# Optimization experiments

Hardware: AMD Instinct MI355X
Metric: run time of the kernel (lower is better)

Reference implementation:

```python
import jax, jax.numpy as jnp
import numpy as np

EPS = 1e-5

def bn(x, g, b):
    # BatchNorm1d, training-mode batch statistics.
    axes = (0, 2) if x.ndim == 3 else (0,)
    m = jnp.mean(x, axis=axes, keepdims=True)
    v = jnp.var(x, axis=axes, keepdims=True)
    shape = (1, -1, 1) if x.ndim == 3 else (1, -1)
    return (x - m) / jnp.sqrt(v + EPS) * g.reshape(shape) + b.reshape(shape)

def conv1(x, w):
    # 1x1 conv1d == channel matmul: w [O,C], x [B,C,N]
    return jnp.einsum('oc,bcn->bon', w, x)

def knn_cov(x, local_idx, k):
    # x: [B,C,N], local_idx: [B,N] bool (local=True branch)
    B, C, N = x.shape
    xx = jnp.sum(x * x, axis=1, keepdims=True)          # [B,1,N]
    inner = -2.0 * jnp.einsum('bcn,bcm->bnm', x, x)      # [B,N,N]
    pd = -xx - inner - jnp.swapaxes(xx, 1, 2)            # neg sq dist [B,N,N]
    Min = jnp.min(pd, axis=-1)                           # [B,N]
    pd = jnp.where(local_idx[:, None, :], pd, Min[:, :, None])
    idx = jax.lax.top_k(jax.lax.stop_gradient(pd), k)[1]  # [B,N,k] nearest
    pts = jnp.swapaxes(x, 1, 2)                          # [B,N,C]
    knn_x = jax.vmap(lambda p, i: p[i])(pts, idx)        # [B,N,k,C]
    knn_x = knn_x - jnp.mean(knn_x, axis=2, keepdims=True)
    cov = jnp.einsum('bnkc,bnkd->bncd', knn_x, knn_x)    # [B,N,C,C]
    cov = cov.reshape(B, N, C * C).transpose(0, 2, 1)    # [B,C^2,N]
    return jnp.concatenate([x, cov], axis=1)             # [B,C+C^2,N]

def setup_inputs() -> dict:
    key = jax.random.key(0)
    ks = jax.random.split(key, 16)
    B, C, N, k = 4, 3, 8192, 20
    emb = 1024
    d = {}
    d['x'] = jax.random.normal(ks[0], (B, C, N), dtype=jnp.float32)
    d['local_idx'] = jax.random.randint(ks[1], (B, N), 0, 2) > 0
    d['k'] = k
    cin = C + C * C  # 12
    d['w1'] = jax.random.normal(ks[2], (64, cin), jnp.float32) * 0.1
    d['w2'] = jax.random.normal(ks[3], (64, 64), jnp.float32) * 0.1
    d['w3'] = jax.random.normal(ks[4], (64, 64), jnp.float32) * 0.1
    d['w4'] = jax.random.normal(ks[5], (128, 64), jnp.float32) * 0.1
    d['w5'] = jax.random.normal(ks[6], (emb, 128), jnp.float32) * 0.05
    for i, c in zip(range(1, 6), [64, 64, 64, 128, emb]):
        d[f'g{i}'] = jnp.ones((c,), jnp.float32)
        d[f'b{i}'] = jnp.zeros((c,), jnp.float32)
    d['lw1'] = jax.random.normal(ks[7], (512, emb), jnp.float32) * 0.03
    d['g6'] = jnp.ones((512,), jnp.float32)
    d['b6'] = jnp.zeros((512,), jnp.float32)
    d['lw2'] = jax.random.normal(ks[8], (4, 512), jnp.float32) * 0.05
    d['lb2'] = jnp.zeros((4,), jnp.float32)
    return d

def reference(x, local_idx, k, w1, w2, w3, w4, w5,
              g1, b1, g2, b2, g3, b3, g4, b4, g5, b5,
              lw1, g6, b6, lw2, lb2):
    h = knn_cov(x, local_idx, k)                 # [B,12,N]
    h = jax.nn.relu(bn(conv1(h, w1), g1, b1))
    h = jax.nn.relu(bn(conv1(h, w2), g2, b2))
    h = jax.nn.relu(bn(conv1(h, w3), g3, b3))
    h = jax.nn.relu(bn(conv1(h, w4), g4, b4))
    h = jax.nn.relu(bn(conv1(h, w5), g5, b5))    # [B,emb,N]
    h = jnp.max(h, axis=2)                        # global max pool [B,emb]
    h = jax.nn.relu(bn(h @ lw1.T, g6, b6))        # [B,512]
    # dropout: identity at eval
    return h @ lw2.T + lb2                        # [B,4]
```

## Files before the change

kernel.cpp:

```cpp
#include <hip/hip_runtime.h>

constexpr int BB = 4, NN = 8192, KNB = 20;
constexpr int BN_ = BB * NN;
constexpr float EPSV = 1e-5f;

constexpr size_t OFF_MODE  = 0;
constexpr size_t OFF_PCNT  = 16;
constexpr size_t OFF_PL    = 64;
constexpr size_t OFF_M0 = OFF_PL + 131072;
constexpr size_t OFF_S0 = OFF_M0 + 12;
constexpr size_t OFF_M1 = OFF_S0 + 144;
constexpr size_t OFF_S1 = OFF_M1 + 64;
constexpr size_t OFF_M2 = OFF_S1 + 64 * 64;
constexpr size_t OFF_S2 = OFF_M2 + 64;
constexpr size_t OFF_M3 = OFF_S2 + 64 * 64;
constexpr size_t OFF_S3 = OFF_M3 + 64;
constexpr size_t OFF_M4 = OFF_S3 + 64 * 64;
constexpr size_t OFF_S4 = OFF_M4 + 128;
constexpr size_t OFF_POOL = OFF_S4 + 128 * 128;
constexpr size_t OFF_ZEND = OFF_POOL + BB * 1024;
constexpr size_t OFF_A1 = OFF_ZEND;
constexpr size_t OFF_B1 = OFF_A1 + 64;
constexpr size_t OFF_A2 = OFF_B1 + 64;
constexpr size_t OFF_B2 = OFF_A2 + 64;
constexpr size_t OFF_A3 = OFF_B2 + 64;
constexpr size_t OFF_B3 = OFF_A3 + 64;
constexpr size_t OFF_A4 = OFF_B3 + 64;
constexpr size_t OFF_B4 = OFF_A4 + 128;
constexpr size_t OFF_A5 = OFF_B4 + 128;
constexpr size_t OFF_B5 = OFF_A5 + 1024;
constexpr size_t OFF_SH = OFF_B5 + 1024;
constexpr size_t OFF_WT1 = OFF_SH + BB * 512;
constexpr size_t OFF_WT2 = OFF_WT1 + 768;
constexpr size_t OFF_WT3 = OFF_WT2 + 4096;
constexpr size_t OFF_WT4 = OFF_WT3 + 4096;
constexpr size_t OFF_WT5_RAW = OFF_WT4 + 8192;
constexpr size_t OFF_WT5 = (OFF_WT5_RAW + 63) & ~size_t(63);
constexpr size_t OFF_H0_RAW = OFF_WT5 + 1024 * 128;
constexpr size_t OFF_H0 = (OFF_H0_RAW + 63) & ~size_t(63);
constexpr size_t OFF_H1 = OFF_H0 + (size_t)BB * 12 * NN;
constexpr size_t OFF_H2 = OFF_H1 + (size_t)BB * 64 * NN;
constexpr size_t OFF_H3 = OFF_H1;
constexpr size_t OFF_H4 = OFF_H2 + (size_t)BB * 64 * NN;
constexpr size_t OFF_P64  = OFF_H4;
constexpr size_t OFF_P128 = OFF_H1;
constexpr size_t WS_FLOATS = OFF_H4 + (size_t)BB * 128 * NN;

__device__ inline float dist3(const float4 c, float x0, float x1, float x2) {
  const float d0 = c.x - x0, d1 = c.y - x1, d2 = c.z - x2;
  return __builtin_fmaf(d0, d0, __builtin_fmaf(d1, d1, d2 * d2));
}

__global__ __launch_bounds__(256) void k_prep(const unsigned int* __restrict__ li32,
                                              int* __restrict__ mode,
                                              int* __restrict__ pcnt,
                                              float4* __restrict__ pl,
                                              const float* __restrict__ x) {
  const int b = blockIdx.x;
  const int t = threadIdx.x;
  const int lane = t & 63;
  const int w = t >> 6;
  __shared__ int s_wc[4];
  __shared__ int s_base;
  __shared__ int s_any;
  if (t == 0) { s_base = 0; s_any = 0; }
  __syncthreads();
  unsigned int any = 0;
  for (int i = t; i < 2048; i += 256) any |= (li32[b * 2048 + i] > 1u) ? 1u : 0u;
  if (any) atomicOr(&s_any, 1);
  __syncthreads();
  const int md = s_any;
  if (b == 0 && t == 0) *mode = md;
  const unsigned char* p8 = (const unsigned char*)li32;
  const float* __restrict__ xb = x + (size_t)b * 3 * NN;
  for (int j0 = 0; j0 < NN; j0 += 256) {
    const int m = j0 + t;
    const int f = md ? (p8[b * NN + m] != 0) : (li32[b * NN + m] != 0);
    const unsigned long long mask = __ballot(f);
    const int pos = __popcll(mask & ((1ull << lane) - 1ull));
    if (lane == 0) s_wc[w] = (int)__popcll(mask);
    __syncthreads();
    int off = s_base;
    for (int ww = 0; ww < w; ++ww) off += s_wc[ww];
    const int tot = s_wc[0] + s_wc[1] + s_wc[2] + s_wc[3];
    if (f) pl[(size_t)b * NN + off + pos] =
        make_float4(xb[m], xb[NN + m], xb[2 * NN + m], __int_as_float(m));
    __syncthreads();
    if (t == 0) s_base += tot;
    __syncthreads();
  }
  if (t == 0) pcnt[b] = s_base;
}

__global__ void k_wtall(const float* __restrict__ w1, const float* __restrict__ w2,
                        const float* __restrict__ w3, const float* __restrict__ w4,
                        const float* __restrict__ w5, float* __restrict__ wt1,
                        float* __restrict__ wt2, float* __restrict__ wt3,
                        float* __restrict__ wt4, float* __restrict__ wt5) {
  const int i = blockIdx.x * 256 + threadIdx.x;
  if (i < 768)        { const int o = i / 12,  c = i % 12;  wt1[c * 64 + o]  = w1[i]; }
  else if (i < 4864)  { const int j = i - 768;  const int o = j >> 6, c = j & 63;  wt2[c * 64 + o]  = w2[j]; }
  else if (i < 8960)  { const int j = i - 4864; const int o = j >> 6, c = j & 63;  wt3[c * 64 + o]  = w3[j]; }
  else if (i < 17152) { const int j = i - 8960; const int o = j >> 6, c = j & 63;  wt4[c * 128 + o] = w4[j]; }
  else if (i < 148224){ const int j = i - 17152;const int o = j >> 7, c = j & 127; wt5[c * 1024 + o] = w5[j]; }
}

__global__ __launch_bounds__(512) void k_knn(const float* __restrict__ x,
                                             const float4* __restrict__ pl,
                                             const int* __restrict__ pcnt,
                                             float* __restrict__ h0) {
  const int blk  = blockIdx.x;
  const int b    = blk >> 7;
  const int tile = blk & 127;
  const int t    = threadIdx.x;
  const int lane = t & 63;
  const int w    = __builtin_amdgcn_readfirstlane(t >> 6);
  const int n    = tile * 64 + lane;

  __shared__ float s_pool[8 * 64 * 21];
  __shared__ float s_T[64];
  __shared__ float s_red[64][13];
  __shared__ int   s_tc[64];
  __shared__ int   s_ti[64][24];
  float* __restrict__ s_dbuf = s_pool;

  const float* __restrict__ xb  = x + (size_t)b * 3 * NN;
  const float4* __restrict__ plb = pl + (size_t)b * NN;
  const int cnt = pcnt[b];
  const float xn0 = xb[n], xn1 = xb[NN + n], xn2 = xb[2 * NN + n];

  const int jlo = (cnt * w) >> 3;
  const int jhi = (cnt * (w + 1)) >> 3;

  float tk[KNB];
#pragma unroll
  for (int i = 0; i < KNB; ++i) tk[i] = 3.0e38f;

  {
    float thr = 3.0e38f;
    int bc = 0;
    int j = jlo;
    for (; j + 3 < jhi; j += 4) {
      const float4 c0 = plb[j],     c1 = plb[j + 1];
      const float4 c2 = plb[j + 2], c3 = plb[j + 3];
      const float d0 = dist3(c0, xn0, xn1, xn2);
      const float d1 = dist3(c1, xn0, xn1, xn2);
      const float d2 = dist3(c2, xn0, xn1, xn2);
      const float d3 = dist3(c3, xn0, xn1, xn2);
      if (d0 < thr) { s_dbuf[bc * 512 + t] = d0; ++bc; }
      if (d1 < thr) { s_dbuf[bc * 512 + t] = d1; ++bc; }
      if (d2 < thr) { s_dbuf[bc * 512 + t] = d2; ++bc; }
      if (d3 < thr) { s_dbuf[bc * 512 + t] = d3; ++bc; }
      if (__any(bc >= 8)) {
        for (int i = 0; i < bc; ++i) {
          float dv = s_dbuf[i * 512 + t];
          if (dv < tk[KNB - 1]) {
#pragma unroll
            for (int q2 = 0; q2 < KNB; ++q2) {
              const float lo = fminf(tk[q2], dv);
              dv = fmaxf(tk[q2], dv);
              tk[q2] = lo;
            }
          }
        }
        bc = 0;
        thr = tk[KNB - 1];
      }
    }
    for (; j < jhi; ++j) {
      const float4 c = plb[j];
      const float d = dist3(c, xn0, xn1, xn2);
      if (d < thr) { s_dbuf[bc * 512 + t] = d; ++bc; }
    }
    for (int i = 0; i < bc; ++i) {
      float dv = s_dbuf[i * 512 + t];
      if (dv < tk[KNB - 1]) {
#pragma unroll
        for (int q2 = 0; q2 < KNB; ++q2) {
          const float lo = fminf(tk[q2], dv);
          dv = fmaxf(tk[q2], dv);
          tk[q2] = lo;
        }
      }
    }
  }
  __syncthreads();

  {
    const int base = (w * 64 + lane) * 21;
#pragma unroll
    for (int i = 0; i < KNB; ++i) s_pool[base + i] = tk[i];
    s_pool[base + KNB] = 3.0e38f;
  }
  __syncthreads();

  if (w == 0) {
    int i0 = 0, i1 = 0, i2 = 0, i3 = 0, i4 = 0, i5 = 0, i6 = 0, i7 = 0;
    float T = 0.f;
    for (int c = 0; c < KNB; ++c) {
      const float v0 = s_pool[(0 * 64 + lane) * 21 + i0];
      const float v1 = s_pool[(1 * 64 + lane) * 21 + i1];
      const float v2 = s_pool[(2 * 64 + lane) * 21 + i2];
      const float v3 = s_pool[(3 * 64 + lane) * 21 + i3];
      const float v4 = s_pool[(4 * 64 + lane) * 21 + i4];
      const float v5 = s_pool[(5 * 64 + lane) * 21 + i5];
      const float v6 = s_pool[(6 * 64 + lane) * 21 + i6];
      const float v7 = s_pool[(7 * 64 + lane) * 21 + i7];
      float best = fminf(fminf(fminf(v0, v1), fminf(v2, v3)),
                         fminf(fminf(v4, v5), fminf(v6, v7)));
      int adv, taken;
      adv = (v0 == best) ? 1 : 0;           i0 += adv; taken = adv;
      adv = (!taken && v1 == best) ? 1 : 0; i1 += adv; taken |= adv;
      adv = (!taken && v2 == best) ? 1 : 0; i2 += adv; taken |= adv;
      adv = (!taken && v3 == best) ? 1 : 0; i3 += adv; taken |= adv;
      adv = (!taken && v4 == best) ? 1 : 0; i4 += adv; taken |= adv;
      adv = (!taken && v5 == best) ? 1 : 0; i5 += adv; taken |= adv;
      adv = (!taken && v6 == best) ? 1 : 0; i6 += adv; taken |= adv;
      adv = (!taken && v7 == best) ? 1 : 0; i7 += adv;
      T = best;
    }
    s_T[lane] = T;
    s_tc[lane] = 0;
  }
  __syncthreads();
  const float T = s_T[lane];

  float sx = 0, sy = 0, sz = 0;
  float xx = 0, xy = 0, xz = 0, yy = 0, yz = 0, zz = 0;
  float clf = 0;
  {
    int j = jlo;
    for (; j + 3 < jhi; j += 4) {
      const float4 c0 = plb[j],     c1 = plb[j + 1];
      const float4 c2 = plb[j + 2], c3 = plb[j + 3];
      const float d0 = dist3(c0, xn0, xn1, xn2);
      const float d1 = dist3(c1, xn0, xn1, xn2);
      const float d2 = dist3(c2, xn0, xn1, xn2);
      const float d3 = dist3(c3, xn0, xn1, xn2);
      if (d0 < T) {
        clf += 1.f; sx += c0.x; sy += c0.y; sz += c0.z;
        xx = __builtin_fmaf(c0.x, c0.x, xx); xy = __builtin_fmaf(c0.x, c0.y, xy);
        xz = __builtin_fmaf(c0.x, c0.z, xz); yy = __builtin_fmaf(c0.y, c0.y, yy);
        yz = __builtin_fmaf(c0.y, c0.z, yz); zz = __builtin_fmaf(c0.z, c0.z, zz);
      } else if (d0 == T) {
        const int pos = atomicAdd(&s_tc[lane], 1);
        if (pos < 24) s_ti[lane][pos] = j;
      }
      if (d1 < T) {
        clf += 1.f; sx += c1.x; sy += c1.y; sz += c1.z;
        xx = __builtin_fmaf(c1.x, c1.x, xx); xy = __builtin_fmaf(c1.x, c1.y, xy);
        xz = __builtin_fmaf(c1.x, c1.z, xz); yy = __builtin_fmaf(c1.y, c1.y, yy);
        yz = __builtin_fmaf(c1.y, c1.z, yz); zz = __builtin_fmaf(c1.z, c1.z, zz);
      } else if (d1 == T) {
        const int pos = atomicAdd(&s_tc[lane], 1);
        if (pos < 24) s_ti[lane][pos] = j + 1;
      }
      if (d2 < T) {
        clf += 1.f; sx += c2.x; sy += c2.y; sz += c2.z;
        xx = __builtin_fmaf(c2.x, c2.x, xx); xy = __builtin_fmaf(c2.x, c2.y, xy);
        xz = __builtin_fmaf(c2.x, c2.z, xz); yy = __builtin_fmaf(c2.y, c2.y, yy);
        yz = __builtin_fmaf(c2.y, c2.z, yz); zz = __builtin_fmaf(c2.z, c2.z, zz);
      } else if (d2 == T) {
        const int pos = atomicAdd(&s_tc[lane], 1);
        if (pos < 24) s_ti[lane][pos] = j + 2;
      }
      if (d3 < T) {
        clf += 1.f; sx += c3.x; sy += c3.y; sz += c3.z;
        xx = __builtin_fmaf(c3.x, c3.x, xx); xy = __builtin_fmaf(c3.x, c3.y, xy);
        xz = __builtin_fmaf(c3.x, c3.z, xz); yy = __builtin_fmaf(c3.y, c3.y, yy);
        yz = __builtin_fmaf(c3.y, c3.z, yz); zz = __builtin_fmaf(c3.z, c3.z, zz);
      } else if (d3 == T) {
        const int pos = atomicAdd(&s_tc[lane], 1);
        if (pos < 24) s_ti[lane][pos] = j + 3;
      }
    }
    for (; j < jhi; ++j) {
      const float4 c = plb[j];
      const float d = dist3(c, xn0, xn1, xn2);
      if (d < T) {
        clf += 1.f; sx += c.x; sy += c.y; sz += c.z;
        xx = __builtin_fmaf(c.x, c.x, xx); xy = __builtin_fmaf(c.x, c.y, xy);
        xz = __builtin_fmaf(c.x, c.z, xz); yy = __builtin_fmaf(c.y, c.y, yy);
        yz = __builtin_fmaf(c.y, c.z, yz); zz = __builtin_fmaf(c.z, c.z, zz);
      } else if (d == T) {
        const int pos = atomicAdd(&s_tc[lane], 1);
        if (pos < 24) s_ti[lane][pos] = j;
      }
    }
  }
  __syncthreads();
  {
    const int base = (w * 64 + lane) * 13;
    s_pool[base + 0] = sx; s_pool[base + 1] = sy; s_pool[base + 2] = sz;
    s_pool[base + 3] = xx; s_pool[base + 4] = xy; s_pool[base + 5] = xz;
    s_pool[base + 6] = yy; s_pool[base + 7] = yz; s_pool[base + 8] = zz;
    s_pool[base + 9] = clf;
  }
  __syncthreads();
  {
    const int q = t & 63, a = t >> 6;
    float s = 0.f;
#pragma unroll
    for (int wv = 0; wv < 8; ++wv) s += s_pool[(wv * 64 + q) * 13 + a];
    s_red[q][a] = s;
    if (a < 2) {
      const int a2 = a + 8;
      float s2 = 0.f;
#pragma unroll
      for (int wv = 0; wv < 8; ++wv) s2 += s_pool[(wv * 64 + q) * 13 + a2];
      s_red[q][a2] = s2;
    }
  }
  __syncthreads();

  if (w == 0) {
    float fsx = s_red[lane][0], fsy = s_red[lane][1], fsz = s_red[lane][2];
    float fxx = s_red[lane][3], fxy = s_red[lane][4], fxz = s_red[lane][5];
    float fyy = s_red[lane][6], fyz = s_red[lane][7], fzz = s_red[lane][8];
    const int cl = (int)s_red[lane][9];
    const int r = KNB - cl;
    const int tc = min(s_tc[lane], 24);
    int kk = cl;
    int prev = -1;
    for (int s = 0; s < r; ++s) {
      int best = 0x7fffffff;
      for (int u = 0; u < tc; ++u) {
        const int mi2 = s_ti[lane][u];
        if (mi2 > prev && mi2 < best) best = mi2;
      }
      if (best == 0x7fffffff) break;
      const float4 pp = plb[best];
      fsx += pp.x; fsy += pp.y; fsz += pp.z;
      fxx = __builtin_fmaf(pp.x, pp.x, fxx);
      fxy = __builtin_fmaf(pp.x, pp.y, fxy);
      fxz = __builtin_fmaf(pp.x, pp.z, fxz);
      fyy = __builtin_fmaf(pp.y, pp.y, fyy);
      fyz = __builtin_fmaf(pp.y, pp.z, fyz);
      fzz = __builtin_fmaf(pp.z, pp.z, fzz);
      prev = best;
      ++kk;
    }
    const float kf = (float)max(kk, 1);
    const float inv = 1.0f / kf;
    const float mx = fsx * inv, my = fsy * inv, mz = fsz * inv;
    const float c00 = fxx - kf * mx * mx;
    const float c01 = fxy - kf * mx * my;
    const float c02 = fxz - kf * mx * mz;
    const float c11 = fyy - kf * my * my;
    const float c12 = fyz - kf * my * mz;
    const float c22 = fzz - kf * mz * mz;
    float* __restrict__ op = h0 + (size_t)b * 12 * NN + n;
    op[0] = xn0; op[(size_t)NN] = xn1; op[(size_t)2 * NN] = xn2;
    op[(size_t)3 * NN] = c00; op[(size_t)4 * NN]  = c01; op[(size_t)5 * NN]  = c02;
    op[(size_t)6 * NN] = c01; op[(size_t)7 * NN]  = c11; op[(size_t)8 * NN]  = c12;
    op[(size_t)9 * NN] = c02; op[(size_t)10 * NN] = c12; op[(size_t)11 * NN] = c22;
  }
}

template <int C>
__global__ __launch_bounds__(256) void k_stats_small(const float* __restrict__ h,
                                                     float* __restrict__ mo,
                                                     float* __restrict__ So) {
  constexpr int NP  = C * (C + 1) / 2;
  constexpr int KPT = (NP + 255) / 256;
  __shared__ float tile[C][65];
  const int t = threadIdx.x;
  float acc[KPT];
#pragma unroll
  for (int e = 0; e < KPT; ++e) acc[e] = 0.f;
  float accm = 0.f;
  for (int tl = blockIdx.x; tl < BN_ / 64; tl += gridDim.x) {
    const int b  = tl >> 7;
    const int p0 = (tl & 127) * 64;
    for (int idx = t; idx < C * 64; idx += 256) {
      const int c = idx >> 6, p = idx & 63;
      tile[c][p] = h[((size_t)b * C + c) * NN + p0 + p];
    }
    __syncthreads();
    {
      int ii = 0, rem = t;
#pragma unroll
      for (int e = 0; e < KPT; ++e) {
        const int lin = t + 256 * e;
        if (lin < NP) {
          while (rem >= C - ii) { rem -= C - ii; ++ii; }
          const int jj = ii + rem;
          float s = 0.f;
#pragma unroll 8
          for (int p = 0; p < 64; ++p) s = __builtin_fmaf(tile[ii][p], tile[jj][p], s);
          acc[e] += s;
        }
        rem += 256;
      }
    }
    if (t < C) {
      float s = 0.f;
#pragma unroll 8
      for (int p = 0; p < 64; ++p) s += tile[t][p];
      accm += s;
    }
    __syncthreads();
  }
  {
    int ii = 0, rem = t;
#pragma unroll
    for (int e = 0; e < KPT; ++e) {
      const int lin = t + 256 * e;
      if (lin < NP) {
        while (rem >= C - ii) { rem -= C - ii; ++ii; }
        atomicAdd(&So[ii * C + ii + rem], acc[e]);
      }
      rem += 256;
    }
  }
  if (t < C) atomicAdd(&mo[t], accm);
}

template <int C>
__global__ __launch_bounds__(512) void k_stats(const float* __restrict__ h,
                                               float* __restrict__ part) {
  constexpr int G      = (C == 128) ? 8 : 4;
  constexpr int NPB    = 136 * G * G;
  constexpr int ROWLEN = NPB + C;
  constexpr int STR    = C + 4;
  __shared__ float ht[128][STR];
  __shared__ float red[136][G * G];
  const int t   = threadIdx.x;
  const int blk = blockIdx.x;
  const int b   = blk >> 6;
  const int p0  = (blk & 63) * 128;
  for (int i = t; i < C * 128; i += 512) {
    const int c = i >> 7, p = i & 127;
    ht[p][c] = h[((size_t)b * C + c) * NN + p0 + p];
  }
  __syncthreads();
  const int s  = t >> 8;
  const int pb = t & 255;
  const int bi = pb & 15;
  const int bj = pb >> 4;
  const bool act = (bi <= bj);
  float acc[G * G];
#pragma unroll
  for (int g = 0; g < G * G; ++g) acc[g] = 0.f;
  if (act) {
    for (int p = s * 64; p < s * 64 + 64; ++p) {
      float a[G], bv[G];
      *(float4*)&a[0] = *(const float4*)&ht[p][bi * G];
      *(float4*)&bv[0] = *(const float4*)&ht[p][bj * G];
      if constexpr (G == 8) {
        *(float4*)&a[4] = *(const float4*)&ht[p][bi * G + 4];
        *(float4*)&bv[4] = *(const float4*)&ht[p][bj * G + 4];
      }
#pragma unroll
      for (int gi = 0; gi < G; ++gi)
#pragma unroll
        for (int gj = 0; gj < G; ++gj)
          acc[gi * G + gj] = __builtin_fmaf(a[gi], bv[gj], acc[gi * G + gj]);
    }
  }
  const int rank = bj * (bj + 1) / 2 + bi;
  if (s == 1 && act) {
#pragma unroll
    for (int g = 0; g < G * G; ++g) red[rank][g] = acc[g];
  }
  __syncthreads();
  float* __restrict__ prow = part + (size_t)blk * ROWLEN;
  if (s == 0 && act) {
#pragma unroll
    for (int g = 0; g < G * G; g += 4) {
      float4 v;
      v.x = acc[g + 0] + red[rank][g + 0];
      v.y = acc[g + 1] + red[rank][g + 1];
      v.z = acc[g + 2] + red[rank][g + 2];
      v.w = acc[g + 3] + red[rank][g + 3];
      *(float4*)&prow[rank * G * G + g] = v;
    }
  }
  if (t < C) {
    float sm = 0.f;
#pragma unroll 8
    for (int p = 0; p < 128; ++p) sm += ht[p][t];
    prow[NPB + t] = sm;
  }
}

template <int C>
__global__ __launch_bounds__(256) void k_sred(const float* __restrict__ part,
                                              float* __restrict__ mo,
                                              float* __restrict__ So) {
  constexpr int G      = (C == 128) ? 8 : 4;
  constexpr int GG     = G * G;
  constexpr int NPB    = 136 * GG;
  constexpr int ROWLEN = NPB + C;
  const int e = blockIdx.x * 256 + threadIdx.x;
  if (e >= ROWLEN) return;
  const float* __restrict__ p = part + e;
  float s = 0.f;
#pragma unroll 8
  for (int r = 0; r < 256; ++r) s += p[(size_t)r * ROWLEN];
  if (e < NPB) {
    const int rank = e / GG;
    const int g    = e - rank * GG;
    int bj = 0;
    while ((bj + 1) * (bj + 2) / 2 <= rank) ++bj;
    const int bi = rank - bj * (bj + 1) / 2;
    const int gi = g / G, gj = g - gi * G;
    So[(bi * G + gi) * C + (bj * G + gj)] = s;
  } else {
    mo[e - NPB] = s;
  }
}

template <int CIN, int COUT>
__global__ __launch_bounds__(256) void k_solve(const float* __restrict__ w, const float* __restrict__ g,
                        const float* __restrict__ bb, const float* __restrict__ m,
                        const float* __restrict__ S, float* __restrict__ A,
                        float* __restrict__ Bc) {
  const int wv   = threadIdx.x >> 6;
  const int lane = threadIdx.x & 63;
  const int o    = blockIdx.x * 4 + wv;
  if (o >= COUT) return;
  const float* __restrict__ wr = w + (size_t)o * CIN;
  float mu = 0.f;
  for (int i = lane; i < CIN; i += 64) mu = __builtin_fmaf(wr[i], m[i], mu);
  float e2 = 0.f;
#pragma unroll 4
  for (int lin = lane; lin < CIN * CIN; lin += 64) {
    const int i = lin / CIN;
    const int j = lin - i * CIN;
    const int lo = min(i, j), hi = max(i, j);
    e2 = __builtin_fmaf(wr[i] * wr[j], S[lo * CIN + hi], e2);
  }
#pragma unroll
  for (int off = 32; off >= 1; off >>= 1) {
    mu += __shfl_xor(mu, off, 64);
    e2 += __shfl_xor(e2, off, 64);
  }
  if (lane == 0) {
    mu *= (1.0f / BN_);
    e2 *= (1.0f / BN_);
    const float var = e2 - mu * mu;
    const float a = g[o] / sqrtf(var + EPSV);
    A[o] = a;
    Bc[o] = bb[o] - mu * a;
  }
}

template <int CIN, int COUT>
__global__ __launch_bounds__(256) void k_cgemm(const float* __restrict__ hin,
                                               const float* __restrict__ wt,
                                               const float* __restrict__ A,
                                               const float* __restrict__ Bc,
                                               float* __restrict__ outp) {
  constexpr int nOT = COUT / 64;
  __shared__ float tin[CIN][64];
  __shared__ float twt[CIN][64];
  const int blk = blockIdx.x;
  const int ot  = blk % nOT;
  const int pt  = blk / nOT;
  const int b   = pt >> 7;
  const int p0  = (pt & 127) * 64;
  const int o0  = ot * 64;
  const int t   = threadIdx.x;

  for (int i = t; i < CIN * 16; i += 256) {
    const int c = i >> 4, sgm = i & 15;
    *(float4*)&tin[c][sgm * 4] =
        *(const float4*)&hin[((size_t)b * CIN + c) * NN + p0 + sgm * 4];
    *(float4*)&twt[c][sgm * 4] =
        *(const float4*)&wt[(size_t)c * COUT + o0 + sgm * 4];
  }
  __syncthreads();

  const int to = t & 15;
  const int tp = t >> 4;
  float acc[4][4];
#pragma unroll
  for (int i = 0; i < 4; ++i)
#pragma unroll
    for (int j = 0; j < 4; ++j) acc[i][j] = 0.f;

#pragma unroll 4
  for (int c = 0; c < CIN; ++c) {
    const float4 av = *(const float4*)&twt[c][to * 4];
    const float4 pv = *(const float4*)&tin[c][tp * 4];
    const float aa[4] = {av.x, av.y, av.z, av.w};
    const float pp[4] = {pv.x, pv.y, pv.z, pv.w};
#pragma unroll
    for (int i = 0; i < 4; ++i)
#pragma unroll
      for (int j = 0; j < 4; ++j)
        acc[i][j] = __builtin_fmaf(aa[i], pp[j], acc[i][j]);
  }

#pragma unroll
  for (int i = 0; i < 4; ++i) {
    const int o = o0 + to * 4 + i;
    const float Ao = A[o], Bo = Bc[o];
    float4 vv;
    vv.x = fmaxf(__builtin_fmaf(acc[i][0], Ao, Bo), 0.f);
    vv.y = fmaxf(__builtin_fmaf(acc[i][1], Ao, Bo), 0.f);
    vv.z = fmaxf(__builtin_fmaf(acc[i][2], Ao, Bo), 0.f);
    vv.w = fmaxf(__builtin_fmaf(acc[i][3], Ao, Bo), 0.f);
    *(float4*)&outp[((size_t)b * COUT + o) * NN + p0 + tp * 4] = vv;
  }
}

__global__ __launch_bounds__(256) void k_cgemm5(const float* __restrict__ h4,
                                                const float* __restrict__ wt,
                                                const float* __restrict__ A,
                                                const float* __restrict__ Bc,
                                                float* __restrict__ pooled) {
  __shared__ float tin[64][128];
  __shared__ float twt[64][128];
  const int blk = blockIdx.x;
  const int ot  = blk & 7;
  const int pt  = blk >> 3;
  const int b   = pt >> 6;
  const int p0  = (pt & 63) * 128;
  const int o0  = ot * 128;
  const int t   = threadIdx.x;
  const int to  = t & 15;
  const int tp  = t >> 4;

  float acc[8][8];
#pragma unroll
  for (int i = 0; i < 8; ++i)
#pragma unroll
    for (int j = 0; j < 8; ++j) acc[i][j] = 0.f;

  for (int kc = 0; kc < 128; kc += 64) {
    if (kc) __syncthreads();
    for (int i = t; i < 64 * 32; i += 256) {
      const int c = i >> 5, sg = i & 31;
      *(float4*)&tin[c][sg * 4] =
          *(const float4*)&h4[((size_t)b * 128 + kc + c) * NN + p0 + sg * 4];
      *(float4*)&twt[c][sg * 4] =
          *(const float4*)&wt[(size_t)(kc + c) * 1024 + o0 + sg * 4];
    }
    __syncthreads();
#pragma unroll 2
    for (int c = 0; c < 64; ++c) {
      float w8[8], p8[8];
      *(float4*)&w8[0] = *(const float4*)&twt[c][to * 8];
      *(float4*)&w8[4] = *(const float4*)&twt[c][to * 8 + 4];
      *(float4*)&p8[0] = *(const float4*)&tin[c][tp * 8];
      *(float4*)&p8[4] = *(const float4*)&tin[c][tp * 8 + 4];
#pragma unroll
      for (int i = 0; i < 8; ++i)
#pragma unroll
        for (int j = 0; j < 8; ++j)
          acc[i][j] = __builtin_fmaf(w8[i], p8[j], acc[i][j]);
    }
  }

  float mx[8];
#pragma unroll
  for (int i = 0; i < 8; ++i) {
    const int o = o0 + to * 8 + i;
    const float a = A[o], bo = Bc[o];
    float m = 0.f;
#pragma unroll
    for (int j = 0; j < 8; ++j)
      m = fmaxf(m, __builtin_fmaf(acc[i][j], a, bo));
    m = fmaxf(m, 0.f);
    m = fmaxf(m, __shfl_xor(m, 16, 64));
    m = fmaxf(m, __shfl_xor(m, 32, 64));
    mx[i] = m;
  }
  float* s_part = &twt[0][0];
  __syncthreads();
  const int lane = t & 63, w = t >> 6;
  if (lane < 16) {
#pragma unroll
    for (int i = 0; i < 8; ++i) s_part[w * 128 + to * 8 + i] = mx[i];
  }
  __syncthreads();
  if (t < 128) {
    const float mm = fmaxf(fmaxf(s_part[t], s_part[128 + t]),
                           fmaxf(s_part[256 + t], s_part[384 + t]));
    atomicMax((int*)pooled + (size_t)b * 1024 + o0 + t, __float_as_int(mm));
  }
}

__global__ __launch_bounds__(256) void k_head1(const float* __restrict__ pooled, const float* __restrict__ lw1,
                        const float* __restrict__ g6, const float* __restrict__ b6,
                        float* __restrict__ sh) {
  const int wv   = threadIdx.x >> 6;
  const int lane = threadIdx.x & 63;
  const int o    = blockIdx.x * 4 + wv;
  const float* __restrict__ wr = lw1 + (size_t)o * 1024;
  float y0 = 0, y1 = 0, y2 = 0, y3 = 0;
  for (int c = lane; c < 1024; c += 64) {
    const float wvv = wr[c];
    y0 = __builtin_fmaf(wvv, pooled[c], y0);
    y1 = __builtin_fmaf(wvv, pooled[1024 + c], y1);
    y2 = __builtin_fmaf(wvv, pooled[2048 + c], y2);
    y3 = __builtin_fmaf(wvv, pooled[3072 + c], y3);
  }
#pragma unroll
  for (int off = 32; off >= 1; off >>= 1) {
    y0 += __shfl_xor(y0, off, 64);
    y1 += __shfl_xor(y1, off, 64);
    y2 += __shfl_xor(y2, off, 64);
    y3 += __shfl_xor(y3, off, 64);
  }
  if (lane == 0) {
    const float mu = 0.25f * (y0 + y1 + y2 + y3);
    const float d0 = y0 - mu, d1 = y1 - mu, d2 = y2 - mu, d3 = y3 - mu;
    const float var = 0.25f * (d0 * d0 + d1 * d1 + d2 * d2 + d3 * d3);
    const float a = g6[o] / sqrtf(var + EPSV);
    const float bc = b6[o];
    sh[o]        = fmaxf(__builtin_fmaf(d0, a, bc), 0.f);
    sh[512 + o]  = fmaxf(__builtin_fmaf(d1, a, bc), 0.f);
    sh[1024 + o] = fmaxf(__builtin_fmaf(d2, a, bc), 0.f);
    sh[1536 + o] = fmaxf(__builtin_fmaf(d3, a, bc), 0.f);
  }
}

__global__ void k_head2(const float* __restrict__ sh, const float* __restrict__ lw2,
                        const float* __restrict__ lb2, float* __restrict__ out) {
  const int wv   = threadIdx.x >> 6;
  const int lane = threadIdx.x & 63;
  float s0 = 0, s1 = 0, s2 = 0, s3 = 0;
  for (int c = lane; c < 512; c += 64) {
    const float h = sh[wv * 512 + c];
    s0 = __builtin_fmaf(lw2[c], h, s0);
    s1 = __builtin_fmaf(lw2[512 + c], h, s1);
    s2 = __builtin_fmaf(lw2[1024 + c], h, s2);
    s3 = __builtin_fmaf(lw2[1536 + c], h, s3);
  }
#pragma unroll
  for (int off = 32; off >= 1; off >>= 1) {
    s0 += __shfl_xor(s0, off, 64);
    s1 += __shfl_xor(s1, off, 64);
    s2 += __shfl_xor(s2, off, 64);
    s3 += __shfl_xor(s3, off, 64);
  }
  if (lane == 0) {
    out[wv * 4 + 0] = s0 + lb2[0];
    out[wv * 4 + 1] = s1 + lb2[1];
    out[wv * 4 + 2] = s2 + lb2[2];
    out[wv * 4 + 3] = s3 + lb2[3];
  }
}

extern "C" void kernel_launch(void* const* d_in, const int* in_sizes, int n_in,
                              void* d_out, int out_size, void* d_ws, size_t ws_size,
                              hipStream_t stream) {
  (void)in_sizes; (void)n_in; (void)out_size; (void)ws_size;
  const float* x    = (const float*)d_in[0];
  const void*  lidx = d_in[1];
  const float* w1 = (const float*)d_in[3];
  const float* w2 = (const float*)d_in[4];
  const float* w3 = (const float*)d_in[5];
  const float* w4 = (const float*)d_in[6];
  const float* w5 = (const float*)d_in[7];
  const float* g1 = (const float*)d_in[8],  *b1 = (const float*)d_in[9];
  const float* g2 = (const float*)d_in[10], *b2 = (const float*)d_in[11];
  const float* g3 = (const float*)d_in[12], *b3 = (const float*)d_in[13];
  const float* g4 = (const float*)d_in[14], *b4 = (const float*)d_in[15];
  const float* g5 = (const float*)d_in[16], *b5 = (const float*)d_in[17];
  const float* lw1 = (const float*)d_in[18];
  const float* g6 = (const float*)d_in[19], *b6 = (const float*)d_in[20];
  const float* lw2 = (const float*)d_in[21], *lb2 = (const float*)d_in[22];
  float* out = (float*)d_out;
  float* ws  = (float*)d_ws;

  hipMemsetAsync(ws + OFF_M0, 0, (OFF_ZEND - OFF_M0) * sizeof(float), stream);

  k_prep<<<4, 256, 0, stream>>>((const unsigned int*)lidx, (int*)(ws + OFF_MODE),
                                (int*)(ws + OFF_PCNT), (float4*)(ws + OFF_PL), x);
  k_wtall<<<579, 256, 0, stream>>>(w1, w2, w3, w4, w5, ws + OFF_WT1, ws + OFF_WT2,
                                   ws + OFF_WT3, ws + OFF_WT4, ws + OFF_WT5);
  k_knn<<<512, 512, 0, stream>>>(x, (const float4*)(ws + OFF_PL),
                                 (const int*)(ws + OFF_PCNT), ws + OFF_H0);

  k_stats_small<12><<<128, 256, 0, stream>>>(ws + OFF_H0, ws + OFF_M0, ws + OFF_S0);
  k_solve<12, 64><<<16, 256, 0, stream>>>(w1, g1, b1, ws + OFF_M0, ws + OFF_S0,
                                          ws + OFF_A1, ws + OFF_B1);
  k_cgemm<12, 64><<<512, 256, 0, stream>>>(ws + OFF_H0, ws + OFF_WT1,
                                           ws + OFF_A1, ws + OFF_B1, ws + OFF_H1);

  k_stats<64><<<256, 512, 0, stream>>>(ws + OFF_H1, ws + OFF_P64);
  k_sred<64><<<9, 256, 0, stream>>>(ws + OFF_P64, ws + OFF_M1, ws + OFF_S1);
  k_solve<64, 64><<<16, 256, 0, stream>>>(w2, g2, b2, ws + OFF_M1, ws + OFF_S1,
                                          ws + OFF_A2, ws + OFF_B2);
  k_cgemm<64, 64><<<512, 256, 0, stream>>>(ws + OFF_H1, ws + OFF_WT2,
                                           ws + OFF_A2, ws + OFF_B2, ws + OFF_H2);

  k_stats<64><<<256, 512, 0, stream>>>(ws + OFF_H2, ws + OFF_P64);
  k_sred<64><<<9, 256, 0, stream>>>(ws + OFF_P64, ws + OFF_M2, ws + OFF_S2);
  k_solve<64, 64><<<16, 256, 0, stream>>>(w3, g3, b3, ws + OFF_M2, ws + OFF_S2,
                                          ws + OFF_A3, ws + OFF_B3);
  k_cgemm<64, 64><<<512, 256, 0, stream>>>(ws + OFF_H2, ws + OFF_WT3,
                                           ws + OFF_A3, ws + OFF_B3, ws + OFF_H3);

  k_stats<64><<<256, 512, 0, stream>>>(ws + OFF_H3, ws + OFF_P64);
  k_sred<64><<<9, 256, 0, stream>>>(ws + OFF_P64, ws + OFF_M3, ws + OFF_S3);
  k_solve<64, 128><<<32, 256, 0, stream>>>(w4, g4, b4, ws + OFF_M3, ws + OFF_S3,
                                           ws + OFF_A4, ws + OFF_B4);
  k_cgemm<64, 128><<<1024, 256, 0, stream>>>(ws + OFF_H3, ws + OFF_WT4,
                                             ws + OFF_A4, ws + OFF_B4, ws + OFF_H4);

  k_stats<128><<<256, 512, 0, stream>>>(ws + OFF_H4, ws + OFF_P128);
  k_sred<128><<<35, 256, 0, stream>>>(ws + OFF_P128, ws + OFF_M4, ws + OFF_S4);
  k_solve<128, 1024><<<256, 256, 0, stream>>>(w5, g5, b5, ws + OFF_M4, ws + OFF_S4,
                                              ws + OFF_A5, ws + OFF_B5);
  k_cgemm5<<<2048, 256, 0, stream>>>(ws + OFF_H4, ws + OFF_WT5,
                                     ws + OFF_A5, ws + OFF_B5, ws + OFF_POOL);

  k_head1<<<128, 256, 0, stream>>>(ws + OFF_POOL, lw1, g6, b6, ws + OFF_SH);
  k_head2<<<1, 256, 0, stream>>>(ws + OFF_SH, lw2, lb2, out);
}
```

Measured before the change: 550.2 us.

## Fuse Gram/sum statistics into 64-channel conv GEMM epilogues

```diff
diff --git a/kernel.cpp b/kernel.cpp
--- a/kernel.cpp
+++ b/kernel.cpp
@@ -484,7 +484,7 @@
   }
 }
 
-template <int C>
+template <int C, int NPART>
 __global__ __launch_bounds__(256) void k_sred(const float* __restrict__ part,
                                               float* __restrict__ mo,
                                               float* __restrict__ So) {
@@ -497,7 +497,7 @@
   const float* __restrict__ p = part + e;
   float s = 0.f;
 #pragma unroll 8
-  for (int r = 0; r < 256; ++r) s += p[(size_t)r * ROWLEN];
+  for (int r = 0; r < NPART; ++r) s += p[(size_t)r * ROWLEN];
   if (e < NPB) {
     const int rank = e / GG;
     const int g    = e - rank * GG;
@@ -546,15 +546,18 @@
   }
 }
 
-template <int CIN, int COUT>
+template <int CIN, int COUT, bool GRAM>
 __global__ __launch_bounds__(256) void k_cgemm(const float* __restrict__ hin,
                                                const float* __restrict__ wt,
                                                const float* __restrict__ A,
                                                const float* __restrict__ Bc,
-                                               float* __restrict__ outp) {
+                                               float* __restrict__ outp,
+                                               float* __restrict__ part) {
   constexpr int nOT = COUT / 64;
-  __shared__ float tin[CIN][64];
-  __shared__ float twt[CIN][64];
+  constexpr int POOLSZ = (2 * CIN * 64 > 64 * 68) ? (2 * CIN * 64) : (64 * 68);
+  __shared__ float pool[POOLSZ];
+  float (*tin)[64] = (float(*)[64])pool;
+  float (*twt)[64] = (float(*)[64])(pool + CIN * 64);
   const int blk = blockIdx.x;
   const int ot  = blk % nOT;
   const int pt  = blk / nOT;
@@ -593,16 +596,61 @@
         acc[i][j] = __builtin_fmaf(aa[i], pp[j], acc[i][j]);
   }
 
+  float v[4][4];
 #pragma unroll
   for (int i = 0; i < 4; ++i) {
     const int o = o0 + to * 4 + i;
     const float Ao = A[o], Bo = Bc[o];
     float4 vv;
-    vv.x = fmaxf(__builtin_fmaf(acc[i][0], Ao, Bo), 0.f);
-    vv.y = fmaxf(__builtin_fmaf(acc[i][1], Ao, Bo), 0.f);
-    vv.z = fmaxf(__builtin_fmaf(acc[i][2], Ao, Bo), 0.f);
-    vv.w = fmaxf(__builtin_fmaf(acc[i][3], Ao, Bo), 0.f);
+    vv.x = v[i][0] = fmaxf(__builtin_fmaf(acc[i][0], Ao, Bo), 0.f);
+    vv.y = v[i][1] = fmaxf(__builtin_fmaf(acc[i][1], Ao, Bo), 0.f);
+    vv.z = v[i][2] = fmaxf(__builtin_fmaf(acc[i][2], Ao, Bo), 0.f);
+    vv.w = v[i][3] = fmaxf(__builtin_fmaf(acc[i][3], Ao, Bo), 0.f);
     *(float4*)&outp[((size_t)b * COUT + o) * NN + p0 + tp * 4] = vv;
+  }
+
+  if constexpr (GRAM) {
+    static_assert(COUT == 64, "gram fusion requires block-owned channels");
+    __syncthreads();
+    float* vt = pool;
+#pragma unroll
+    for (int i = 0; i < 4; ++i)
+#pragma unroll
+      for (int j = 0; j < 4; ++j)
+        vt[(tp * 4 + j) * 68 + to * 4 + i] = v[i][j];
+    __syncthreads();
+    const int bi = t & 15;
+    const int bj = t >> 4;
+    float* __restrict__ prow = part + (size_t)blk * 2240;
+    if (bi <= bj) {
+      float g[16];
+#pragma unroll
+      for (int q = 0; q < 16; ++q) g[q] = 0.f;
+      for (int p = 0; p < 64; ++p) {
+        const float4 av = *(const float4*)&vt[p * 68 + bi * 4];
+        const float4 bv = *(const float4*)&vt[p * 68 + bj * 4];
+        const float a4[4] = {av.x, av.y, av.z, av.w};
+        const float b4[4] = {bv.x, bv.y, bv.z, bv.w};
+#pragma unroll
+        for (int gi = 0; gi < 4; ++gi)
+#pragma unroll
+          for (int gj = 0; gj < 4; ++gj)
+            g[gi * 4 + gj] = __builtin_fmaf(a4[gi], b4[gj], g[gi * 4 + gj]);
+      }
+      const int rank = bj * (bj + 1) / 2 + bi;
+#pragma unroll
+      for (int q = 0; q < 16; q += 4) {
+        float4 w4v;
+        w4v.x = g[q + 0]; w4v.y = g[q + 1]; w4v.z = g[q + 2]; w4v.w = g[q + 3];
+        *(float4*)&prow[rank * 16 + q] = w4v;
+      }
+    }
+    if (t < 64) {
+      float sm = 0.f;
+#pragma unroll 8
+      for (int p = 0; p < 64; ++p) sm += vt[p * 68 + t];
+      prow[2176 + t] = sm;
+    }
   }
 }
 
@@ -779,32 +827,33 @@
   k_stats_small<12><<<128, 256, 0, stream>>>(ws + OFF_H0, ws + OFF_M0, ws + OFF_S0);
   k_solve<12, 64><<<16, 256, 0, stream>>>(w1, g1, b1, ws + OFF_M0, ws + OFF_S0,
                                           ws + OFF_A1, ws + OFF_B1);
-  k_cgemm<12, 64><<<512, 256, 0, stream>>>(ws + OFF_H0, ws + OFF_WT1,
-                                           ws + OFF_A1, ws + OFF_B1, ws + OFF_H1);
-
-  k_stats<64><<<256, 512, 0, stream>>>(ws + OFF_H1, ws + OFF_P64);
-  k_sred<64><<<9, 256, 0, stream>>>(ws + OFF_P64, ws + OFF_M1, ws + OFF_S1);
+  k_cgemm<12, 64, true><<<512, 256, 0, stream>>>(ws + OFF_H0, ws + OFF_WT1,
+                                                 ws + OFF_A1, ws + OFF_B1,
+                                                 ws + OFF_H1, ws + OFF_P64);
+
+  k_sred<64, 512><<<9, 256, 0, stream>>>(ws + OFF_P64, ws + OFF_M1, ws + OFF_S1);
   k_solve<64, 64><<<16, 256, 0, stream>>>(w2, g2, b2, ws + OFF_M1, ws + OFF_S1,
                                           ws + OFF_A2, ws + OFF_B2);
-  k_cgemm<64, 64><<<512, 256, 0, stream>>>(ws + OFF_H1, ws + OFF_WT2,
-                                           ws + OFF_A2, ws + OFF_B2, ws + OFF_H2);
-
-  k_stats<64><<<256, 512, 0, stream>>>(ws + OFF_H2, ws + OFF_P64);
-  k_sred<64><<<9, 256, 0, stream>>>(ws + OFF_P64, ws + OFF_M2, ws + OFF_S2);
+  k_cgemm<64, 64, true><<<512, 256, 0, stream>>>(ws + OFF_H1, ws + OFF_WT2,
+                                                 ws + OFF_A2, ws + OFF_B2,
+                                                 ws + OFF_H2, ws + OFF_P64);
+
+  k_sred<64, 512><<<9, 256, 0, stream>>>(ws + OFF_P64, ws + OFF_M2, ws + OFF_S2);
   k_solve<64, 64><<<16, 256, 0, stream>>>(w3, g3, b3, ws + OFF_M2, ws + OFF_S2,
                                           ws + OFF_A3, ws + OFF_B3);
-  k_cgemm<64, 64><<<512, 256, 0, stream>>>(ws + OFF_H2, ws + OFF_WT3,
-                                           ws + OFF_A3, ws + OFF_B3, ws + OFF_H3);
-
-  k_stats<64><<<256, 512, 0, stream>>>(ws + OFF_H3, ws + OFF_P64);
-  k_sred<64><<<9, 256, 0, stream>>>(ws + OFF_P64, ws + OFF_M3, ws + OFF_S3);
+  k_cgemm<64, 64, true><<<512, 256, 0, stream>>>(ws + OFF_H2, ws + OFF_WT3,
+                                                 ws + OFF_A3, ws + OFF_B3,
+                                                 ws + OFF_H3, ws + OFF_P64);
+
+  k_sred<64, 512><<<9, 256, 0, stream>>>(ws + OFF_P64, ws + OFF_M3, ws + OFF_S3);
   k_solve<64, 128><<<32, 256, 0, stream>>>(w4, g4, b4, ws + OFF_M3, ws + OFF_S3,
                                            ws + OFF_A4, ws + OFF_B4);
-  k_cgemm<64, 128><<<1024, 256, 0, stream>>>(ws + OFF_H3, ws + OFF_WT4,
-                                             ws + OFF_A4, ws + OFF_B4, ws + OFF_H4);
+  k_cgemm<64, 128, false><<<1024, 256, 0, stream>>>(ws + OFF_H3, ws + OFF_WT4,
+                                                    ws + OFF_A4, ws + OFF_B4,
+                                                    ws + OFF_H4, nullptr);
 
   k_stats<128><<<256, 512, 0, stream>>>(ws + OFF_H4, ws + OFF_P128);
-  k_sred<128><<<35, 256, 0, stream>>>(ws + OFF_P128, ws + OFF_M4, ws + OFF_S4);
+  k_sred<128, 256><<<35, 256, 0, stream>>>(ws + OFF_P128, ws + OFF_M4, ws + OFF_S4);
   k_solve<128, 1024><<<256, 256, 0, stream>>>(w5, g5, b5, ws + OFF_M4, ws + OFF_S4,
                                               ws + OFF_A5, ws + OFF_B5);
   k_cgemm5<<<2048, 256, 0, stream>>>(ws + OFF_H4, ws + OFF_WT5,
```

Result: slower. 572.5 us (+4.1%).

## Track neighbor indices in top-k to skip second distance pass

Applied to the files above, without the earlier changes.

```diff
diff --git a/kernel.cpp b/kernel.cpp
--- a/kernel.cpp
+++ b/kernel.cpp
@@ -118,6 +118,7 @@
   const int n    = tile * 64 + lane;
 
   __shared__ float s_pool[8 * 64 * 21];
+  __shared__ int   s_dbufi[12 * 512];
   __shared__ float s_T[64];
   __shared__ float s_red[64][13];
   __shared__ int   s_tc[64];
@@ -133,8 +134,9 @@
   const int jhi = (cnt * (w + 1)) >> 3;
 
   float tk[KNB];
-#pragma unroll
-  for (int i = 0; i < KNB; ++i) tk[i] = 3.0e38f;
+  int   ti[KNB];
+#pragma unroll
+  for (int i = 0; i < KNB; ++i) { tk[i] = 3.0e38f; ti[i] = 0; }
 
   {
     float thr = 3.0e38f;
@@ -147,19 +149,23 @@
       const float d1 = dist3(c1, xn0, xn1, xn2);
       const float d2 = dist3(c2, xn0, xn1, xn2);
       const float d3 = dist3(c3, xn0, xn1, xn2);
-      if (d0 < thr) { s_dbuf[bc * 512 + t] = d0; ++bc; }
-      if (d1 < thr) { s_dbuf[bc * 512 + t] = d1; ++bc; }
-      if (d2 < thr) { s_dbuf[bc * 512 + t] = d2; ++bc; }
-      if (d3 < thr) { s_dbuf[bc * 512 + t] = d3; ++bc; }
+      if (d0 < thr) { s_dbuf[bc * 512 + t] = d0; s_dbufi[bc * 512 + t] = j;     ++bc; }
+      if (d1 < thr) { s_dbuf[bc * 512 + t] = d1; s_dbufi[bc * 512 + t] = j + 1; ++bc; }
+      if (d2 < thr) { s_dbuf[bc * 512 + t] = d2; s_dbufi[bc * 512 + t] = j + 2; ++bc; }
+      if (d3 < thr) { s_dbuf[bc * 512 + t] = d3; s_dbufi[bc * 512 + t] = j + 3; ++bc; }
       if (__any(bc >= 8)) {
         for (int i = 0; i < bc; ++i) {
           float dv = s_dbuf[i * 512 + t];
+          int   iv = s_dbufi[i * 512 + t];
           if (dv < tk[KNB - 1]) {
 #pragma unroll
             for (int q2 = 0; q2 < KNB; ++q2) {
-              const float lo = fminf(tk[q2], dv);
-              dv = fmaxf(tk[q2], dv);
-              tk[q2] = lo;
+              const bool lt = dv < tk[q2];
+              const float nd = lt ? tk[q2] : dv;
+              const int   ni = lt ? ti[q2] : iv;
+              tk[q2] = lt ? dv : tk[q2];
+              ti[q2] = lt ? iv : ti[q2];
+              dv = nd; iv = ni;
             }
           }
         }
@@ -170,16 +176,20 @@
     for (; j < jhi; ++j) {
       const float4 c = plb[j];
       const float d = dist3(c, xn0, xn1, xn2);
-      if (d < thr) { s_dbuf[bc * 512 + t] = d; ++bc; }
+      if (d < thr) { s_dbuf[bc * 512 + t] = d; s_dbufi[bc * 512 + t] = j; ++bc; }
     }
     for (int i = 0; i < bc; ++i) {
       float dv = s_dbuf[i * 512 + t];
+      int   iv = s_dbufi[i * 512 + t];
       if (dv < tk[KNB - 1]) {
 #pragma unroll
         for (int q2 = 0; q2 < KNB; ++q2) {
-          const float lo = fminf(tk[q2], dv);
-          dv = fmaxf(tk[q2], dv);
-          tk[q2] = lo;
+          const bool lt = dv < tk[q2];
+          const float nd = lt ? tk[q2] : dv;
+          const int   ni = lt ? ti[q2] : iv;
+          tk[q2] = lt ? dv : tk[q2];
+          ti[q2] = lt ? iv : ti[q2];
+          dv = nd; iv = ni;
         }
       }
     }
@@ -228,64 +238,18 @@
   float sx = 0, sy = 0, sz = 0;
   float xx = 0, xy = 0, xz = 0, yy = 0, yz = 0, zz = 0;
   float clf = 0;
-  {
-    int j = jlo;
-    for (; j + 3 < jhi; j += 4) {
-      const float4 c0 = plb[j],     c1 = plb[j + 1];
-      const float4 c2 = plb[j + 2], c3 = plb[j + 3];
-      const float d0 = dist3(c0, xn0, xn1, xn2);
-      const float d1 = dist3(c1, xn0, xn1, xn2);
-      const float d2 = dist3(c2, xn0, xn1, xn2);
-      const float d3 = dist3(c3, xn0, xn1, xn2);
-      if (d0 < T) {
-        clf += 1.f; sx += c0.x; sy += c0.y; sz += c0.z;
-        xx = __builtin_fmaf(c0.x, c0.x, xx); xy = __builtin_fmaf(c0.x, c0.y, xy);
-        xz = __builtin_fmaf(c0.x, c0.z, xz); yy = __builtin_fmaf(c0.y, c0.y, yy);
-        yz = __builtin_fmaf(c0.y, c0.z, yz); zz = __builtin_fmaf(c0.z, c0.z, zz);
-      } else if (d0 == T) {
-        const int pos = atomicAdd(&s_tc[lane], 1);
-        if (pos < 24) s_ti[lane][pos] = j;
-      }
-      if (d1 < T) {
-        clf += 1.f; sx += c1.x; sy += c1.y; sz += c1.z;
-        xx = __builtin_fmaf(c1.x, c1.x, xx); xy = __builtin_fmaf(c1.x, c1.y, xy);
-        xz = __builtin_fmaf(c1.x, c1.z, xz); yy = __builtin_fmaf(c1.y, c1.y, yy);
-        yz = __builtin_fmaf(c1.y, c1.z, yz); zz = __builtin_fmaf(c1.z, c1.z, zz);
-      } else if (d1 == T) {
-        const int pos = atomicAdd(&s_tc[lane], 1);
-        if (pos < 24) s_ti[lane][pos] = j + 1;
-      }
-      if (d2 < T) {
-        clf += 1.f; sx += c2.x; sy += c2.y; sz += c2.z;
-        xx = __builtin_fmaf(c2.x, c2.x, xx); xy = __builtin_fmaf(c2.x, c2.y, xy);
-        xz = __builtin_fmaf(c2.x, c2.z, xz); yy = __builtin_fmaf(c2.y, c2.y, yy);
-        yz = __builtin_fmaf(c2.y, c2.z, yz); zz = __builtin_fmaf(c2.z, c2.z, zz);
-      } else if (d2 == T) {
-        const int pos = atomicAdd(&s_tc[lane], 1);
-        if (pos < 24) s_ti[lane][pos] = j + 2;
-      }
-      if (d3 < T) {
-        clf += 1.f; sx += c3.x; sy += c3.y; sz += c3.z;
-        xx = __builtin_fmaf(c3.x, c3.x, xx); xy = __builtin_fmaf(c3.x, c3.y, xy);
-        xz = __builtin_fmaf(c3.x, c3.z, xz); yy = __builtin_fmaf(c3.y, c3.y, yy);
-        yz = __builtin_fmaf(c3.y, c3.z, yz); zz = __builtin_fmaf(c3.z, c3.z, zz);
-      } else if (d3 == T) {
-        const int pos = atomicAdd(&s_tc[lane], 1);
-        if (pos < 24) s_ti[lane][pos] = j + 3;
-      }
-    }
-    for (; j < jhi; ++j) {
-      const float4 c = plb[j];
-      const float d = dist3(c, xn0, xn1, xn2);
-      if (d < T) {
-        clf += 1.f; sx += c.x; sy += c.y; sz += c.z;
-        xx = __builtin_fmaf(c.x, c.x, xx); xy = __builtin_fmaf(c.x, c.y, xy);
-        xz = __builtin_fmaf(c.x, c.z, xz); yy = __builtin_fmaf(c.y, c.y, yy);
-        yz = __builtin_fmaf(c.y, c.z, yz); zz = __builtin_fmaf(c.z, c.z, zz);
-      } else if (d == T) {
-        const int pos = atomicAdd(&s_tc[lane], 1);
-        if (pos < 24) s_ti[lane][pos] = j;
-      }
+#pragma unroll
+  for (int i = 0; i < KNB; ++i) {
+    const float d = tk[i];
+    if (d < T) {
+      const float4 c = plb[ti[i]];
+      clf += 1.f; sx += c.x; sy += c.y; sz += c.z;
+      xx = __builtin_fmaf(c.x, c.x, xx); xy = __builtin_fmaf(c.x, c.y, xy);
+      xz = __builtin_fmaf(c.x, c.z, xz); yy = __builtin_fmaf(c.y, c.y, yy);
+      yz = __builtin_fmaf(c.y, c.z, yz); zz = __builtin_fmaf(c.z, c.z, zz);
+    } else if (d == T) {
+      const int pos = atomicAdd(&s_tc[lane], 1);
+      if (pos < 24) s_ti[lane][pos] = ti[i];
     }
   }
   __syncthreads();
```

Result: slower. 593.0 us (+7.8%).
